# Optimization experiments

Measured on AMD Instinct MI355X. Metric: run time of the kernel, lower is better.

Reference implementation:

```python
import jax, jax.numpy as jnp
import numpy as np

H = 128  # hidden_dim

def _lstm_step(h, c, x, Wih, Whh, bih, bhh):
    # PyTorch gate order: i, f, g, o
    gates = x @ Wih.T + h @ Whh.T + (bih + bhh)  # (B, 4H)
    i, f, g, o = jnp.split(gates, 4, axis=-1)
    c = jax.nn.sigmoid(f) * c + jax.nn.sigmoid(i) * jnp.tanh(g)
    h = jax.nn.sigmoid(o) * jnpp_tanh(c) if False else jax.nn.sigmoid(o) * jnp.tanh(c)
    return h, c

def _lstm_layer(x_seq, h0, c0, Wih, Whh, bih, bhh):
    # x_seq: (B, T, D) -> scan over time
    def step(carry, x_t):
        h, c = _lstm_step(carry[0], carry[1], x_t, Wih, Whh, bih, bhh)
        return (h, c), h
    (h, c), ys = jax.lax.scan(step, (h0, c0), jnp.swapaxes(x_seq, 0, 1))
    return jnp.swapaxes(ys, 0, 1), h, c  # (B,T,H), (B,H), (B,H)

def _mk_params(key):
    s = 1.0 / np.sqrt(H)
    names_shapes = [
        ('enc_Wih0', (4*H, 7)), ('enc_Whh0', (4*H, H)), ('enc_bih0', (4*H,)), ('enc_bhh0', (4*H,)),
        ('enc_Wih1', (4*H, H)), ('enc_Whh1', (4*H, H)), ('enc_bih1', (4*H,)), ('enc_bhh1', (4*H,)),
        ('dec_Wih0', (4*H, 2)), ('dec_Whh0', (4*H, H)), ('dec_bih0', (4*H,)), ('dec_bhh0', (4*H,)),
        ('dec_Wih1', (4*H, H)), ('dec_Whh1', (4*H, H)), ('dec_bih1', (4*H,)), ('dec_bhh1', (4*H,)),
        ('out_W', (2, H)), ('out_b', (2,)),
    ]
    params = {}
    for i, (n, shp) in enumerate(names_shapes):
        params[n] = jax.random.uniform(jax.random.fold_in(key, i), shp, jnp.float32, -s, s)
    return params

def setup_inputs() -> dict:
    key = jax.random.key(0)
    inp = {
        'target': jax.random.normal(jax.random.fold_in(key, 100), (65536, 20, 7), jnp.float32),
        'neigh_dyn': jnp.zeros((1,), jnp.float32),
        'neigh_spatial': jnp.zeros((1,), jnp.float32),
        'lane': jnp.zeros((1,), jnp.float32),
    }
    inp.update(_mk_params(key))
    return inp

def reference(target, neigh_dyn, neigh_spatial, lane,
              enc_Wih0, enc_Whh0, enc_bih0, enc_bhh0,
              enc_Wih1, enc_Whh1, enc_bih1, enc_bhh1,
              dec_Wih0, dec_Whh0, dec_bih0, dec_bhh0,
              dec_Wih1, dec_Whh1, dec_bih1, dec_bhh1,
              out_W, out_b):
    B = target.shape[0]
    pred_len = 25
    z = jnp.zeros((B, H), target.dtype)
    # encoder: 2 stacked LSTM layers (eval mode, no dropout)
    y0, h0, c0 = _lstm_layer(target, z, z, enc_Wih0, enc_Whh0, enc_bih0, enc_bhh0)
    y1, h1, c1 = _lstm_layer(y0, z, z, enc_Wih1, enc_Whh1, enc_bih1, enc_bhh1)
    def dec_step(carry, _):
        dh0, dc0, dh1, dc1, x = carry
        dh0, dc0 = _lstm_step(dh0, dc0, x, dec_Wih0, dec_Whh0, dec_bih0, dec_bhh0)
        dh1, dc1 = _lstm_step(dh1, dc1, dh0, dec_Wih1, dec_Whh1, dec_bih1, dec_bhh1)
        pred = dh1 @ out_W.T + out_b  # (B, 2)
        return (dh0, dc0, dh1, dc1, pred), pred
    init = (h0, c0, h1, c1, jnp.zeros((B, 2), target.dtype))
    _, preds = jax.lax.scan(dec_step, init, None, length=pred_len)  # (pred_len, B, 2)
    return jnp.swapaxes(preds, 0, 1)  # (B, pred_len, 2)
```

## Files before the change

kernel.cpp:

```cpp
#include <hip/hip_runtime.h>
#include <math.h>

typedef unsigned short u16;
typedef __attribute__((ext_vector_type(8))) short bf16x8;
typedef __attribute__((ext_vector_type(4))) float f32x4;

#define TENC 20
#define TDEC 25
#define MTB 32
#define HSTR 136
#define XSTRD 40

#define W_E0IH 0
#define W_E0HH 32768
#define W_E1IH 163840
#define W_E1HH 294912
#define W_D0IH 425984
#define W_D0HH 458752
#define W_D1IH 589824
#define W_D1HH 720896
#define W_TOTAL 851968
#define BIAS_BYTE_OFF (W_TOTAL*2)

__device__ __forceinline__ void split16(float v, u16& hi, u16& lo) {
  unsigned int u = __float_as_uint(v);
  hi = (u16)(u >> 16);
  float hif = __uint_as_float(u & 0xffff0000u);
  lo = (u16)(__float_as_uint(v - hif) >> 16);
}

__global__ void prep_kernel(
    const float* __restrict__ e0ih, const float* __restrict__ e0hh,
    const float* __restrict__ e1ih, const float* __restrict__ e1hh,
    const float* __restrict__ d0ih, const float* __restrict__ d0hh,
    const float* __restrict__ d1ih, const float* __restrict__ d1hh,
    const float* __restrict__ be0i, const float* __restrict__ be0h,
    const float* __restrict__ be1i, const float* __restrict__ be1h,
    const float* __restrict__ bd0i, const float* __restrict__ bd0h,
    const float* __restrict__ bd1i, const float* __restrict__ bd1h,
    u16* __restrict__ wsw, float* __restrict__ wsb)
{
  int idx = blockIdx.x * blockDim.x + threadIdx.x;
  if (idx < W_TOTAL) {
    const float* src; int K, nkt, off;
    if (idx < W_E0HH)      { src=e0ih; K=7;   nkt=1; off=W_E0IH; }
    else if (idx < W_E1IH) { src=e0hh; K=128; nkt=4; off=W_E0HH; }
    else if (idx < W_E1HH) { src=e1ih; K=128; nkt=4; off=W_E1IH; }
    else if (idx < W_D0IH) { src=e1hh; K=128; nkt=4; off=W_E1HH; }
    else if (idx < W_D0HH) { src=d0ih; K=2;   nkt=1; off=W_D0IH; }
    else if (idx < W_D1IH) { src=d0hh; K=128; nkt=4; off=W_D0HH; }
    else if (idx < W_D1HH) { src=d1ih; K=128; nkt=4; off=W_D1IH; }
    else                   { src=d1hh; K=128; nkt=4; off=W_D1HH; }
    int n = idx - off;
    int pass_sz = nkt * 16384;
    int pass = n / pass_sz; n -= pass * pass_sz;
    int kt = n >> 14;
    int r  = n & 16383;
    int t = r >> 12;
    int w = (r >> 9) & 7;
    int l = (r >> 3) & 63;
    int j = r & 7;
    int k  = kt*32 + (l >> 4)*8 + j;
    int ng = t*128 + w*16 + (l & 15);
    float v = (k < K) ? src[ng*K + k] : 0.0f;
    u16 hi, lo; split16(v, hi, lo);
    wsw[idx] = (pass == 0) ? hi : lo;
  } else if (idx < W_TOTAL + 2048) {
    int b = idx - W_TOTAL;
    int set = b >> 9, r = b & 511;
    int t = r & 3, hl = (r >> 2) & 15, w = r >> 6;
    int n = t*128 + w*16 + hl;
    float v;
    if      (set == 0) v = be0i[n] + be0h[n];
    else if (set == 1) v = be1i[n] + be1h[n];
    else if (set == 2) v = bd0i[n] + bd0h[n];
    else               v = bd1i[n] + bd1h[n];
    wsb[b] = v;
  }
}

__device__ __forceinline__ float sigm(float x) { return 1.0f / (1.0f + __expf(-x)); }
__device__ __forceinline__ float tanh_f(float x) {
  float e = __expf(2.0f * x);
  return 1.0f - 2.0f / (e + 1.0f);
}

template<int NKT>
__device__ __forceinline__ void gemm_frag(f32x4 acc[2][4],
    const u16* Ahi, const u16* Alo, const int astride,
    const u16* __restrict__ Wf, int w, int l)
{
  const int g = l >> 4, hl = l & 15;
  #pragma unroll
  for (int kt = 0; kt < NKT; ++kt) {
    const int kb = kt*32 + g*8;
    bf16x8 ah0 = *(const bf16x8*)(Ahi + hl*astride + kb);
    bf16x8 ah1 = *(const bf16x8*)(Ahi + (16 + hl)*astride + kb);
    bf16x8 al0 = *(const bf16x8*)(Alo + hl*astride + kb);
    bf16x8 al1 = *(const bf16x8*)(Alo + (16 + hl)*astride + kb);
    #pragma unroll
    for (int t = 0; t < 4; ++t) {
      const u16* wp = Wf + (((kt*4 + t)*8 + w)*64 + l)*8;
      bf16x8 bh = *(const bf16x8*)(wp);
      bf16x8 bl = *(const bf16x8*)(wp + NKT*16384);
      acc[0][t] = __builtin_amdgcn_mfma_f32_16x16x32_bf16(ah0, bh, acc[0][t], 0, 0, 0);
      acc[1][t] = __builtin_amdgcn_mfma_f32_16x16x32_bf16(ah1, bh, acc[1][t], 0, 0, 0);
      acc[0][t] = __builtin_amdgcn_mfma_f32_16x16x32_bf16(ah0, bl, acc[0][t], 0, 0, 0);
      acc[1][t] = __builtin_amdgcn_mfma_f32_16x16x32_bf16(ah1, bl, acc[1][t], 0, 0, 0);
      acc[0][t] = __builtin_amdgcn_mfma_f32_16x16x32_bf16(al0, bh, acc[0][t], 0, 0, 0);
      acc[1][t] = __builtin_amdgcn_mfma_f32_16x16x32_bf16(al1, bh, acc[1][t], 0, 0, 0);
    }
  }
}

template<int NKT_IH>
__device__ __forceinline__ void layer_step(
    const u16* xhi, const u16* xlo, int xstride,
    u16* hhi, u16* hlo,
    const u16* __restrict__ Wih, const u16* __restrict__ Whh,
    const float* __restrict__ biasf,
    float cC[2][4], int w, int l)
{
  const int g = l >> 4, hl = l & 15;
  f32x4 acc[2][4];
  float4 bb = *(const float4*)(biasf + (w*16 + hl)*4);
  const float bv[4] = {bb.x, bb.y, bb.z, bb.w};
  #pragma unroll
  for (int m = 0; m < 2; ++m)
    #pragma unroll
    for (int t = 0; t < 4; ++t) {
      f32x4 a; a[0] = bv[t]; a[1] = bv[t]; a[2] = bv[t]; a[3] = bv[t];
      acc[m][t] = a;
    }
  gemm_frag<NKT_IH>(acc, xhi, xlo, xstride, Wih, w, l);
  gemm_frag<4>(acc, hhi, hlo, HSTR, Whh, w, l);

  __syncthreads();
  #pragma unroll
  for (int m = 0; m < 2; ++m)
    #pragma unroll
    for (int r = 0; r < 4; ++r) {
      float iv = sigm(acc[m][0][r]);
      float fv = sigm(acc[m][1][r]);
      float gv = tanh_f(acc[m][2][r]);
      float ov = sigm(acc[m][3][r]);
      float c  = fv * cC[m][r] + iv * gv;
      cC[m][r] = c;
      float h  = ov * tanh_f(c);
      u16 a_, b_; split16(h, a_, b_);
      int row = m*16 + g*4 + r;
      hhi[row*HSTR + w*16 + hl] = a_;
      hlo[row*HSTR + w*16 + hl] = b_;
    }
  __syncthreads();
}

__global__ __launch_bounds__(512) void lstm_main(
    const float* __restrict__ target,
    const u16* __restrict__ wsw, const float* __restrict__ wsb,
    const float* __restrict__ outW, const float* __restrict__ outB,
    float* __restrict__ out)
{
  __shared__ u16 h0hi[32*HSTR], h0lo[32*HSTR];
  __shared__ u16 h1hi[32*HSTR], h1lo[32*HSTR];
  __shared__ u16 xhi[32*XSTRD], xlo[32*XSTRD];
  __shared__ float ps[256];

  const int tid = threadIdx.x;
  const int w = tid >> 6, l = tid & 63;
  const long sbase = (long)blockIdx.x * MTB;

  float c0[2][4], c1[2][4];
  #pragma unroll
  for (int m = 0; m < 2; ++m)
    #pragma unroll
    for (int r = 0; r < 4; ++r) { c0[m][r] = 0.f; c1[m][r] = 0.f; }

  for (int i = tid; i < 32*HSTR; i += 512) { h0hi[i]=0; h0lo[i]=0; h1hi[i]=0; h1lo[i]=0; }
  for (int i = tid; i < 32*XSTRD; i += 512) { xhi[i]=0; xlo[i]=0; }
  __syncthreads();

  for (int t = 0; t < TENC; ++t) {
    {
      int s = tid >> 3, d = tid & 7;
      if (tid < 256 && d < 7) {
        float v = target[(sbase + s)*(TENC*7) + t*7 + d];
        u16 a_, b_; split16(v, a_, b_);
        xhi[s*XSTRD + d] = a_;
        xlo[s*XSTRD + d] = b_;
      }
    }
    __syncthreads();
    layer_step<1>(xhi, xlo, XSTRD, h0hi, h0lo, wsw + W_E0IH, wsw + W_E0HH, wsb + 0,    c0, w, l);
    layer_step<4>(h0hi, h0lo, HSTR, h1hi, h1lo, wsw + W_E1IH, wsw + W_E1HH, wsb + 512, c1, w, l);
  }

  for (int i = tid; i < 32*XSTRD; i += 512) { xhi[i]=0; xlo[i]=0; }
  __syncthreads();
  const float ob0 = outB[0], ob1 = outB[1];

  for (int p = 0; p < TDEC; ++p) {
    layer_step<1>(xhi, xlo, XSTRD, h0hi, h0lo, wsw + W_D0IH, wsw + W_D0HH, wsb + 1024, c0, w, l);
    layer_step<4>(h0hi, h0lo, HSTR, h1hi, h1lo, wsw + W_D1IH, wsw + W_D1HH, wsb + 1536, c1, w, l);

    if (tid < 256) {
      int s = tid & 31, oq = tid >> 5;
      int o = oq & 1, q = oq >> 1;
      const float* wo = outW + o*128 + q*32;
      const u16* phh = h1hi + s*HSTR + q*32;
      const u16* phl = h1lo + s*HSTR + q*32;
      float a = 0.f;
      #pragma unroll 8
      for (int k = 0; k < 32; ++k) {
        float hv = __uint_as_float(((unsigned int)phh[k]) << 16)
                 + __uint_as_float(((unsigned int)phl[k]) << 16);
        a = fmaf(hv, wo[k], a);
      }
      ps[oq*32 + s] = a;
    }
    __syncthreads();
    if (tid < 64) {
      int s = tid & 31, o = tid >> 5;
      float pred = ps[(0+o)*32+s] + ps[(2+o)*32+s] + ps[(4+o)*32+s] + ps[(6+o)*32+s]
                 + (o ? ob1 : ob0);
      out[((sbase + s)*TDEC + p)*2 + o] = pred;
      u16 a_, b_; split16(pred, a_, b_);
      xhi[s*XSTRD + o] = a_;
      xlo[s*XSTRD + o] = b_;
    }
    __syncthreads();
  }
}

extern "C" void kernel_launch(void* const* d_in, const int* in_sizes, int n_in,
                              void* d_out, int out_size, void* d_ws, size_t ws_size,
                              hipStream_t stream)
{
  const float* target = (const float*)d_in[0];
  const float* e0ih=(const float*)d_in[4],  *e0hh=(const float*)d_in[5];
  const float* be0i=(const float*)d_in[6],  *be0h=(const float*)d_in[7];
  const float* e1ih=(const float*)d_in[8],  *e1hh=(const float*)d_in[9];
  const float* be1i=(const float*)d_in[10], *be1h=(const float*)d_in[11];
  const float* d0ih=(const float*)d_in[12], *d0hh=(const float*)d_in[13];
  const float* bd0i=(const float*)d_in[14], *bd0h=(const float*)d_in[15];
  const float* d1ih=(const float*)d_in[16], *d1hh=(const float*)d_in[17];
  const float* bd1i=(const float*)d_in[18], *bd1h=(const float*)d_in[19];
  const float* outW=(const float*)d_in[20], *outB=(const float*)d_in[21];
  u16*   wsw = (u16*)d_ws;
  float* wsb = (float*)((char*)d_ws + BIAS_BYTE_OFF);
  float* out = (float*)d_out;
  const int B = in_sizes[0] / (TENC*7);

  hipLaunchKernelGGL(prep_kernel, dim3((W_TOTAL + 2048 + 255)/256), dim3(256), 0, stream,
      e0ih,e0hh,e1ih,e1hh,d0ih,d0hh,d1ih,d1hh,
      be0i,be0h,be1i,be1h,bd0i,bd0h,bd1i,bd1h, wsw, wsb);
  hipLaunchKernelGGL(lstm_main, dim3(B/MTB), dim3(512), 0, stream,
      target, wsw, wsb, outW, outB, out);
}
```

Before: 9.829 ms.

## Double batch tile to 64 rows and interleave hi/lo weight fragments

```diff
diff --git a/kernel.cpp b/kernel.cpp
--- a/kernel.cpp
+++ b/kernel.cpp
@@ -7,19 +7,19 @@
 
 #define TENC 20
 #define TDEC 25
-#define MTB 32
+#define MTB 64
 #define HSTR 136
 #define XSTRD 40
 
 #define W_E0IH 0
-#define W_E0HH 32768
-#define W_E1IH 163840
-#define W_E1HH 294912
-#define W_D0IH 425984
-#define W_D0HH 458752
-#define W_D1IH 589824
-#define W_D1HH 720896
-#define W_TOTAL 851968
+#define W_E0HH 33280
+#define W_E1IH 164864
+#define W_E1HH 296448
+#define W_D0IH 428032
+#define W_D0HH 461312
+#define W_D1IH 592896
+#define W_D1HH 724480
+#define W_TOTAL 855552
 #define BIAS_BYTE_OFF (W_TOTAL*2)
 
 __device__ __forceinline__ void split16(float v, u16& hi, u16& lo) {
@@ -52,14 +52,14 @@
     else if (idx < W_D1HH) { src=d1ih; K=128; nkt=4; off=W_D1IH; }
     else                   { src=d1hh; K=128; nkt=4; off=W_D1HH; }
     int n = idx - off;
-    int pass_sz = nkt * 16384;
-    int pass = n / pass_sz; n -= pass * pass_sz;
-    int kt = n >> 14;
-    int r  = n & 16383;
-    int t = r >> 12;
-    int w = (r >> 9) & 7;
-    int l = (r >> 3) & 63;
-    int j = r & 7;
+    if (n >= nkt*32768) { wsw[idx] = 0; return; }
+    int kt = n >> 15;
+    int r  = n & 32767;
+    int t   = r >> 13;
+    int w   = (r >> 10) & 7;
+    int l   = (r >> 4) & 63;
+    int j16 = r & 15;
+    int pass = j16 >> 3, j = j16 & 7;
     int k  = kt*32 + (l >> 4)*8 + j;
     int ng = t*128 + w*16 + (l & 15);
     float v = (k < K) ? src[ng*K + k] : 0.0f;
@@ -86,7 +86,7 @@
 }
 
 template<int NKT>
-__device__ __forceinline__ void gemm_frag(f32x4 acc[2][4],
+__device__ __forceinline__ void gemm_frag(f32x4 acc[4][4],
     const u16* Ahi, const u16* Alo, const int astride,
     const u16* __restrict__ Wf, int w, int l)
 {
@@ -94,21 +94,23 @@
   #pragma unroll
   for (int kt = 0; kt < NKT; ++kt) {
     const int kb = kt*32 + g*8;
-    bf16x8 ah0 = *(const bf16x8*)(Ahi + hl*astride + kb);
-    bf16x8 ah1 = *(const bf16x8*)(Ahi + (16 + hl)*astride + kb);
-    bf16x8 al0 = *(const bf16x8*)(Alo + hl*astride + kb);
-    bf16x8 al1 = *(const bf16x8*)(Alo + (16 + hl)*astride + kb);
+    bf16x8 ah[4], al[4];
+    #pragma unroll
+    for (int m = 0; m < 4; ++m) {
+      ah[m] = *(const bf16x8*)(Ahi + (m*16 + hl)*astride + kb);
+      al[m] = *(const bf16x8*)(Alo + (m*16 + hl)*astride + kb);
+    }
     #pragma unroll
     for (int t = 0; t < 4; ++t) {
-      const u16* wp = Wf + (((kt*4 + t)*8 + w)*64 + l)*8;
+      const u16* wp = Wf + (((kt*4 + t)*8 + w)*64 + l)*16;
       bf16x8 bh = *(const bf16x8*)(wp);
-      bf16x8 bl = *(const bf16x8*)(wp + NKT*16384);
-      acc[0][t] = __builtin_amdgcn_mfma_f32_16x16x32_bf16(ah0, bh, acc[0][t], 0, 0, 0);
-      acc[1][t] = __builtin_amdgcn_mfma_f32_16x16x32_bf16(ah1, bh, acc[1][t], 0, 0, 0);
-      acc[0][t] = __builtin_amdgcn_mfma_f32_16x16x32_bf16(ah0, bl, acc[0][t], 0, 0, 0);
-      acc[1][t] = __builtin_amdgcn_mfma_f32_16x16x32_bf16(ah1, bl, acc[1][t], 0, 0, 0);
-      acc[0][t] = __builtin_amdgcn_mfma_f32_16x16x32_bf16(al0, bh, acc[0][t], 0, 0, 0);
-      acc[1][t] = __builtin_amdgcn_mfma_f32_16x16x32_bf16(al1, bh, acc[1][t], 0, 0, 0);
+      bf16x8 bl = *(const bf16x8*)(wp + 8);
+      #pragma unroll
+      for (int m = 0; m < 4; ++m) {
+        acc[m][t] = __builtin_amdgcn_mfma_f32_16x16x32_bf16(ah[m], bh, acc[m][t], 0, 0, 0);
+        acc[m][t] = __builtin_amdgcn_mfma_f32_16x16x32_bf16(ah[m], bl, acc[m][t], 0, 0, 0);
+        acc[m][t] = __builtin_amdgcn_mfma_f32_16x16x32_bf16(al[m], bh, acc[m][t], 0, 0, 0);
+      }
     }
   }
 }
@@ -119,14 +121,14 @@
     u16* hhi, u16* hlo,
     const u16* __restrict__ Wih, const u16* __restrict__ Whh,
     const float* __restrict__ biasf,
-    float cC[2][4], int w, int l)
+    float cC[4][4], int w, int l)
 {
   const int g = l >> 4, hl = l & 15;
-  f32x4 acc[2][4];
+  f32x4 acc[4][4];
   float4 bb = *(const float4*)(biasf + (w*16 + hl)*4);
   const float bv[4] = {bb.x, bb.y, bb.z, bb.w};
   #pragma unroll
-  for (int m = 0; m < 2; ++m)
+  for (int m = 0; m < 4; ++m)
     #pragma unroll
     for (int t = 0; t < 4; ++t) {
       f32x4 a; a[0] = bv[t]; a[1] = bv[t]; a[2] = bv[t]; a[3] = bv[t];
@@ -137,7 +139,7 @@
 
   __syncthreads();
   #pragma unroll
-  for (int m = 0; m < 2; ++m)
+  for (int m = 0; m < 4; ++m)
     #pragma unroll
     for (int r = 0; r < 4; ++r) {
       float iv = sigm(acc[m][0][r]);
@@ -161,41 +163,39 @@
     const float* __restrict__ outW, const float* __restrict__ outB,
     float* __restrict__ out)
 {
-  __shared__ u16 h0hi[32*HSTR], h0lo[32*HSTR];
-  __shared__ u16 h1hi[32*HSTR], h1lo[32*HSTR];
-  __shared__ u16 xhi[32*XSTRD], xlo[32*XSTRD];
-  __shared__ float ps[256];
+  __shared__ u16 h0hi[MTB*HSTR], h0lo[MTB*HSTR];
+  __shared__ u16 h1hi[MTB*HSTR], h1lo[MTB*HSTR];
+  __shared__ u16 xhi[MTB*XSTRD], xlo[MTB*XSTRD];
+  __shared__ float ps[8*MTB];
 
   const int tid = threadIdx.x;
   const int w = tid >> 6, l = tid & 63;
   const long sbase = (long)blockIdx.x * MTB;
 
-  float c0[2][4], c1[2][4];
-  #pragma unroll
-  for (int m = 0; m < 2; ++m)
+  float c0[4][4], c1[4][4];
+  #pragma unroll
+  for (int m = 0; m < 4; ++m)
     #pragma unroll
     for (int r = 0; r < 4; ++r) { c0[m][r] = 0.f; c1[m][r] = 0.f; }
 
-  for (int i = tid; i < 32*HSTR; i += 512) { h0hi[i]=0; h0lo[i]=0; h1hi[i]=0; h1lo[i]=0; }
-  for (int i = tid; i < 32*XSTRD; i += 512) { xhi[i]=0; xlo[i]=0; }
+  for (int i = tid; i < MTB*HSTR; i += 512) { h0hi[i]=0; h0lo[i]=0; h1hi[i]=0; h1lo[i]=0; }
+  for (int i = tid; i < MTB*XSTRD; i += 512) { xhi[i]=0; xlo[i]=0; }
   __syncthreads();
 
   for (int t = 0; t < TENC; ++t) {
-    {
-      int s = tid >> 3, d = tid & 7;
-      if (tid < 256 && d < 7) {
-        float v = target[(sbase + s)*(TENC*7) + t*7 + d];
-        u16 a_, b_; split16(v, a_, b_);
-        xhi[s*XSTRD + d] = a_;
-        xlo[s*XSTRD + d] = b_;
-      }
+    if (tid < 7*MTB) {
+      int s = tid / 7, d = tid - s*7;
+      float v = target[(sbase + s)*(TENC*7) + t*7 + d];
+      u16 a_, b_; split16(v, a_, b_);
+      xhi[s*XSTRD + d] = a_;
+      xlo[s*XSTRD + d] = b_;
     }
     __syncthreads();
     layer_step<1>(xhi, xlo, XSTRD, h0hi, h0lo, wsw + W_E0IH, wsw + W_E0HH, wsb + 0,    c0, w, l);
     layer_step<4>(h0hi, h0lo, HSTR, h1hi, h1lo, wsw + W_E1IH, wsw + W_E1HH, wsb + 512, c1, w, l);
   }
 
-  for (int i = tid; i < 32*XSTRD; i += 512) { xhi[i]=0; xlo[i]=0; }
+  for (int i = tid; i < MTB*XSTRD; i += 512) { xhi[i]=0; xlo[i]=0; }
   __syncthreads();
   const float ob0 = outB[0], ob1 = outB[1];
 
@@ -203,8 +203,8 @@
     layer_step<1>(xhi, xlo, XSTRD, h0hi, h0lo, wsw + W_D0IH, wsw + W_D0HH, wsb + 1024, c0, w, l);
     layer_step<4>(h0hi, h0lo, HSTR, h1hi, h1lo, wsw + W_D1IH, wsw + W_D1HH, wsb + 1536, c1, w, l);
 
-    if (tid < 256) {
-      int s = tid & 31, oq = tid >> 5;
+    {
+      int s = tid & (MTB-1), oq = tid >> 6;
       int o = oq & 1, q = oq >> 1;
       const float* wo = outW + o*128 + q*32;
       const u16* phh = h1hi + s*HSTR + q*32;
@@ -216,12 +216,12 @@
                  + __uint_as_float(((unsigned int)phl[k]) << 16);
         a = fmaf(hv, wo[k], a);
       }
-      ps[oq*32 + s] = a;
+      ps[oq*MTB + s] = a;
     }
     __syncthreads();
-    if (tid < 64) {
-      int s = tid & 31, o = tid >> 5;
-      float pred = ps[(0+o)*32+s] + ps[(2+o)*32+s] + ps[(4+o)*32+s] + ps[(6+o)*32+s]
+    if (tid < 2*MTB) {
+      int s = tid & (MTB-1), o = tid >> 6;
+      float pred = ps[(0+o)*MTB+s] + ps[(2+o)*MTB+s] + ps[(4+o)*MTB+s] + ps[(6+o)*MTB+s]
                  + (o ? ob1 : ob0);
       out[((sbase + s)*TDEC + p)*2 + o] = pred;
       u16 a_, b_; split16(pred, a_, b_);
```

New measurement: 8.291 ms. 1.19x faster.
